# Kernel tuning notes

Hardware: AMD Instinct MI355X
Metric: run time of the kernel (lower is better)

Reference implementation:

```python
import jax, jax.numpy as jnp
import numpy as np

TEMPERATURE = 0.07
NEG = -1e9  # finite stand-in for -inf; exp(-1e9) underflows to 0 in fp32, identical math


def setup_inputs() -> dict:
    key = jax.random.key(0)
    k1, k2 = jax.random.split(key)
    B, D = 8192, 128
    emb = jax.random.normal(k1, (B, D), dtype=jnp.float32)
    emb = emb / jnp.linalg.norm(emb, axis=1, keepdims=True)  # docstring: normalized embeddings
    labels = jax.random.randint(k2, (B,), 0, 2048, dtype=jnp.int64)
    return {"embeddings": emb, "labels": labels}


def reference(embeddings, labels):
    B = labels.shape[0]
    # [B, B] pairwise similarities / temperature
    sim = jnp.matmul(embeddings, embeddings.T) / TEMPERATURE
    eye = jnp.eye(B, dtype=bool)
    sim = jnp.where(eye, NEG, sim)  # mask self-similarity
    # positives: same outfit id, excluding self
    pos_mask = (labels[None, :] == labels[:, None]) & (~eye)
    # row-wise log-softmax (torch code does log_softmax over each row)
    log_probs = jax.nn.log_softmax(sim, axis=1)
    pos_count = jnp.sum(pos_mask, axis=1)  # [B]
    pos_sum = jnp.sum(jnp.where(pos_mask, log_probs, 0.0), axis=1)  # [B]
    has_pos = pos_count > 0
    row_mean = jnp.where(has_pos, pos_sum / jnp.maximum(pos_count, 1), 0.0)
    count = jnp.sum(has_pos)
    loss = -jnp.sum(row_mean) / jnp.maximum(count, 1)
    return loss
```

## Files before the change

kernel.cpp:

```cpp
#include <hip/hip_runtime.h>


#define BATCH 8192
#define DIMK  128
#define INV_T 14.285714285714286f
#define MSUB  14.285714285714286f
#define K1    20.609929155311264f
#define K2    20.609929155311264f

typedef short bf16x8 __attribute__((ext_vector_type(8)));
typedef float f32x4  __attribute__((ext_vector_type(4)));

__device__ __forceinline__ unsigned short f2bf_rne(float f) {
    unsigned u = __float_as_uint(f);
    u += 0x7FFFu + ((u >> 16) & 1u);
    return (unsigned short)(u >> 16);
}
__device__ __forceinline__ float bf2f(unsigned short b) {
    return __uint_as_float(((unsigned)b) << 16);
}

__global__ __launch_bounds__(256) void
prep_kernel(const float* __restrict__ emb, ushort* __restrict__ Ebf,
            float4* __restrict__ zcol4) {
    int i = blockIdx.x * 256 + threadIdx.x;
    if (i < 2048) {
        float4 z = {0.f, 0.f, 0.f, 0.f};
        zcol4[i] = z;
    }
    float4 v = ((const float4*)emb)[i];
    ushort4 o;
    o.x = f2bf_rne(v.x); o.y = f2bf_rne(v.y);
    o.z = f2bf_rne(v.z); o.w = f2bf_rne(v.w);
    ((ushort4*)Ebf)[i] = o;
}

__global__ __launch_bounds__(512) void
contrastive_main(const ushort* __restrict__ Ebf, float* __restrict__ zpartR,
                 float* __restrict__ zcol, const float* __restrict__ emb,
                 const int* __restrict__ labels, float* __restrict__ gsum,
                 int* __restrict__ gcnt) {
    __shared__ __align__(16) ushort Bs[2048 * 8];
    __shared__ float cpart[8][128];
    const int tid  = threadIdx.x;
    const int lane = tid & 63;
    const int wid  = tid >> 6;
    const int quad = lane >> 4;
    const int l16  = lane & 15;

    if (blockIdx.x >= 1056) {
        int* labs = (int*)&Bs[0];
#pragma unroll
        for (int it = 0; it < 4; ++it)
            ((int4*)labs)[it * 512 + tid] = ((const int4*)labels)[it * 512 + tid];
        __syncthreads();

        const int c = (blockIdx.x - 1056) * 8 + wid;
        float2 acc = {0.f, 0.f};
        int cnt = 0;
        int nl = labs[lane];
        for (int j0 = 0; j0 < BATCH; j0 += 64) {
            int cur = nl;
            int nidx = j0 + 64 < BATCH ? j0 + 64 : 0;
            nl = labs[nidx + lane];
            unsigned long long m = __ballot(cur == c);
            cnt += __popcll(m);
            while (m) {
                int j = __ffsll(m) - 1;
                m &= m - 1;
                float2 v = *(const float2*)(emb + (size_t)(j0 + j) * DIMK + lane * 2);
                acc.x += v.x; acc.y += v.y;
            }
        }
        *(float2*)(gsum + (size_t)c * DIMK + lane * 2) = acc;
        if (lane == 0) gcnt[c] = cnt;
        return;
    }

    const int bid = blockIdx.x;
    const int tt  = (bid & 7) * 132 + (bid >> 3);

    int b = tt >> 1;
    const int ch = tt & 1;
    int ti = 0;
    while (b >= 32 - ti) { b -= 32 - ti; ++ti; }
    const int tj  = ti + b;
    const int tj2 = tj * 2 + ch;
    const int row_base = ti * 256 + wid * 32;
    const int col_base = tj * 256 + ch * 128;

    bf16x8 afrag[2][4];
#pragma unroll
    for (int mt = 0; mt < 2; ++mt)
#pragma unroll
        for (int kk = 0; kk < 4; ++kk)
            afrag[mt][kk] = *(const bf16x8*)(Ebf + (size_t)(row_base + mt * 16 + l16) * DIMK
                                             + kk * 32 + quad * 8);

#pragma unroll
    for (int it = 0; it < 4; ++it) {
        int f   = it * 512 + tid;
        int col = f >> 4;
        int c   = f & 15;
        uint4 v = *(const uint4*)(Ebf + (size_t)(col_base + col) * DIMK + c * 8);
        *(uint4*)&Bs[((col >> 4) * 256 + c * 16 + ((col & 15) ^ c)) * 8] = v;
    }
    __syncthreads();

    float zacc[8];
#pragma unroll
    for (int s = 0; s < 8; ++s) zacc[s] = 0.f;

    for (int nt = 0; nt < 8; ++nt) {
        bf16x8 bfrag[4];
#pragma unroll
        for (int kk = 0; kk < 4; ++kk) {
            const int c2 = kk * 4 + quad;
            bfrag[kk] = *(const bf16x8*)&Bs[(nt * 256 + c2 * 16 + (l16 ^ c2)) * 8];
        }

        float csum = 0.f;
#pragma unroll
        for (int mt = 0; mt < 2; ++mt) {
            f32x4 c = {0.f, 0.f, 0.f, 0.f};
#pragma unroll
            for (int kk = 0; kk < 4; ++kk)
                c = __builtin_amdgcn_mfma_f32_16x16x32_bf16(afrag[mt][kk], bfrag[kk], c, 0, 0, 0);
#pragma unroll
            for (int r = 0; r < 4; ++r) {
                float e = __builtin_amdgcn_exp2f(__builtin_fmaf(c[r], K1, -K2));
                zacc[mt * 4 + r] += e;
                csum += e;
            }
        }
        csum += __shfl_xor(csum, 16, 64);
        csum += __shfl_xor(csum, 32, 64);
        if (quad == 0) cpart[wid][nt * 16 + l16] = csum;
    }

#pragma unroll
    for (int s = 0; s < 8; ++s) {
        float z = zacc[s];
#pragma unroll
        for (int m = 1; m <= 8; m <<= 1) z += __shfl_xor(z, m, 64);
        if (l16 == 0) {
            int row = row_base + (s >> 2) * 16 + quad * 4 + (s & 3);
            zpartR[(size_t)row * 64 + tj2] = z;
        }
    }

    __syncthreads();
    if (ti != tj && tid < 128) {
        float s = cpart[0][tid] + cpart[1][tid] + cpart[2][tid] + cpart[3][tid]
                + cpart[4][tid] + cpart[5][tid] + cpart[6][tid] + cpart[7][tid];
        atomicAdd(&zcol[col_base + tid], s);
    }
}

__global__ __launch_bounds__(256) void
finalize1(const float* __restrict__ emb, const ushort* __restrict__ Ebf,
          const int* __restrict__ labels, const float* __restrict__ gsum,
          const int* __restrict__ gcnt, const float* __restrict__ zpartR,
          const float* __restrict__ zcol,
          float* __restrict__ bpart, int* __restrict__ bcnt) {
    __shared__ float sf[4];
    __shared__ int   si[4];
    const int lane = threadIdx.x & 63;
    const int wid  = threadIdx.x >> 6;

    float wsum = 0.f;
    int   wcnt = 0;
#pragma unroll
    for (int it = 0; it < 4; ++it) {
        const int r   = blockIdx.x * 16 + wid * 4 + it;
        const int lab = labels[r];
        const int P   = gcnt[lab] - 1;
        const int tp2 = (r >> 8) * 2;

        float2 ev = *(const float2*)(emb  + (size_t)r   * DIMK + lane * 2);
        float2 gv = *(const float2*)(gsum + (size_t)lab * DIMK + lane * 2);
        unsigned bb = *(const unsigned*)(Ebf + (size_t)r * DIMK + lane * 2);
        float b0 = bf2f((unsigned short)(bb & 0xFFFF));
        float b1 = bf2f((unsigned short)(bb >> 16));

        float dotg = ev.x * gv.x + ev.y * gv.y;
        float ssd  = ev.x * ev.x + ev.y * ev.y;
        float sdbf = b0 * b0 + b1 * b1;
        float Z = 0.f;
        if (lane >= tp2) Z = zpartR[(size_t)r * 64 + lane];

#pragma unroll
        for (int m = 1; m <= 32; m <<= 1) {
            dotg += __shfl_xor(dotg, m, 64);
            ssd  += __shfl_xor(ssd,  m, 64);
            sdbf += __shfl_xor(sdbf, m, 64);
            Z    += __shfl_xor(Z,    m, 64);
        }
        Z += zcol[r];
        Z -= __builtin_amdgcn_exp2f(__builtin_fmaf(sdbf, K1, -K2));

        const bool has = (P > 0);
        wsum += has ? ((dotg - ssd) * INV_T / (float)P - MSUB - __logf(Z)) : 0.f;
        wcnt += has ? 1 : 0;
    }

    if (lane == 0) { sf[wid] = wsum; si[wid] = wcnt; }
    __syncthreads();
    if (threadIdx.x == 0) {
        bpart[blockIdx.x] = sf[0] + sf[1] + sf[2] + sf[3];
        bcnt [blockIdx.x] = si[0] + si[1] + si[2] + si[3];
    }
}

__global__ __launch_bounds__(256) void
finalize2(const float* __restrict__ bpart, const int* __restrict__ bcnt,
          float* __restrict__ out) {
    __shared__ float sf[4];
    __shared__ int   si[4];
    const int t = threadIdx.x;
    float v = 0.f; int c = 0;
#pragma unroll
    for (int k = 0; k < 2; ++k) {
        v += bpart[t + k * 256];
        c += bcnt [t + k * 256];
    }
#pragma unroll
    for (int m = 1; m <= 32; m <<= 1) {
        v += __shfl_xor(v, m, 64);
        c += __shfl_xor(c, m, 64);
    }
    if ((t & 63) == 0) { sf[t >> 6] = v; si[t >> 6] = c; }
    __syncthreads();
    if (t == 0) {
        float tot = sf[0] + sf[1] + sf[2] + sf[3];
        int cc = si[0] + si[1] + si[2] + si[3];
        out[0] = -tot / (float)(cc > 0 ? cc : 1);
    }
}

extern "C" void kernel_launch(void* const* d_in, const int* in_sizes, int n_in,
                              void* d_out, int out_size, void* d_ws, size_t ws_size,
                              hipStream_t stream) {
    const float* emb  = (const float*)d_in[0];
    const int* labels = (const int*)d_in[1];
    float* out        = (float*)d_out;

    char* ws = (char*)d_ws;
    ushort* Ebf    = (ushort*)ws;
    float*  zpartR = (float*)(ws + (2u << 20));
    float*  zcol   = (float*)(ws + (4u << 20));
    float*  gsum   = (float*)(ws + (5u << 20));
    int*    gcnt   = (int*)  (ws + (6u << 20));
    float*  bpart  = (float*)(ws + (6u << 20) + 8192);
    int*    bcnt   = (int*)  (ws + (6u << 20) + 16384);

    prep_kernel<<<1024, 256, 0, stream>>>(emb, Ebf, (float4*)zcol);
    contrastive_main<<<1312, 512, 0, stream>>>(Ebf, zpartR, zcol,
                                               emb, labels, gsum, gcnt);
    finalize1<<<512, 256, 0, stream>>>(emb, Ebf, labels, gsum, gcnt, zpartR, zcol,
                                       bpart, bcnt);
    finalize2<<<1, 256, 0, stream>>>(bpart, bcnt, out);
}
```

Baseline: 93.28 us.

## Fuse bf16 conversion into main kernel and drop prep kernel

New measurement: 97.29 us. 1.04x slower.

```diff
diff --git a/kernel.cpp b/kernel.cpp
--- a/kernel.cpp
+++ b/kernel.cpp
@@ -19,27 +19,19 @@
 __device__ __forceinline__ float bf2f(unsigned short b) {
     return __uint_as_float(((unsigned)b) << 16);
 }
-
-__global__ __launch_bounds__(256) void
-prep_kernel(const float* __restrict__ emb, ushort* __restrict__ Ebf,
-            float4* __restrict__ zcol4) {
-    int i = blockIdx.x * 256 + threadIdx.x;
-    if (i < 2048) {
-        float4 z = {0.f, 0.f, 0.f, 0.f};
-        zcol4[i] = z;
-    }
-    float4 v = ((const float4*)emb)[i];
-    ushort4 o;
-    o.x = f2bf_rne(v.x); o.y = f2bf_rne(v.y);
-    o.z = f2bf_rne(v.z); o.w = f2bf_rne(v.w);
-    ((ushort4*)Ebf)[i] = o;
+__device__ __forceinline__ bf16x8 cvt8(float4 a, float4 b) {
+    bf16x8 o;
+    o[0] = (short)f2bf_rne(a.x); o[1] = (short)f2bf_rne(a.y);
+    o[2] = (short)f2bf_rne(a.z); o[3] = (short)f2bf_rne(a.w);
+    o[4] = (short)f2bf_rne(b.x); o[5] = (short)f2bf_rne(b.y);
+    o[6] = (short)f2bf_rne(b.z); o[7] = (short)f2bf_rne(b.w);
+    return o;
 }
 
 __global__ __launch_bounds__(512) void
-contrastive_main(const ushort* __restrict__ Ebf, float* __restrict__ zpartR,
-                 float* __restrict__ zcol, const float* __restrict__ emb,
-                 const int* __restrict__ labels, float* __restrict__ gsum,
-                 int* __restrict__ gcnt) {
+contrastive_main(const float* __restrict__ emb, const int* __restrict__ labels,
+                 float* __restrict__ zpartR, float* __restrict__ zcol,
+                 float* __restrict__ gsum, int* __restrict__ gcnt) {
     __shared__ __align__(16) ushort Bs[2048 * 8];
     __shared__ float cpart[8][128];
     const int tid  = threadIdx.x;
@@ -93,17 +85,20 @@
 #pragma unroll
     for (int mt = 0; mt < 2; ++mt)
 #pragma unroll
-        for (int kk = 0; kk < 4; ++kk)
-            afrag[mt][kk] = *(const bf16x8*)(Ebf + (size_t)(row_base + mt * 16 + l16) * DIMK
-                                             + kk * 32 + quad * 8);
+        for (int kk = 0; kk < 4; ++kk) {
+            const float* p = emb + (size_t)(row_base + mt * 16 + l16) * DIMK
+                             + kk * 32 + quad * 8;
+            afrag[mt][kk] = cvt8(*(const float4*)p, *(const float4*)(p + 4));
+        }
 
 #pragma unroll
     for (int it = 0; it < 4; ++it) {
         int f   = it * 512 + tid;
         int col = f >> 4;
         int c   = f & 15;
-        uint4 v = *(const uint4*)(Ebf + (size_t)(col_base + col) * DIMK + c * 8);
-        *(uint4*)&Bs[((col >> 4) * 256 + c * 16 + ((col & 15) ^ c)) * 8] = v;
+        const float* p = emb + (size_t)(col_base + col) * DIMK + c * 8;
+        bf16x8 v = cvt8(*(const float4*)p, *(const float4*)(p + 4));
+        *(bf16x8*)&Bs[((col >> 4) * 256 + c * 16 + ((col & 15) ^ c)) * 8] = v;
     }
     __syncthreads();
 
@@ -158,10 +153,9 @@
 }
 
 __global__ __launch_bounds__(256) void
-finalize1(const float* __restrict__ emb, const ushort* __restrict__ Ebf,
-          const int* __restrict__ labels, const float* __restrict__ gsum,
-          const int* __restrict__ gcnt, const float* __restrict__ zpartR,
-          const float* __restrict__ zcol,
+finalize1(const float* __restrict__ emb, const int* __restrict__ labels,
+          const float* __restrict__ gsum, const int* __restrict__ gcnt,
+          const float* __restrict__ zpartR, const float* __restrict__ zcol,
           float* __restrict__ bpart, int* __restrict__ bcnt) {
     __shared__ float sf[4];
     __shared__ int   si[4];
@@ -171,17 +165,16 @@
     float wsum = 0.f;
     int   wcnt = 0;
 #pragma unroll
-    for (int it = 0; it < 4; ++it) {
-        const int r   = blockIdx.x * 16 + wid * 4 + it;
+    for (int it = 0; it < 2; ++it) {
+        const int r   = blockIdx.x * 8 + wid * 2 + it;
         const int lab = labels[r];
         const int P   = gcnt[lab] - 1;
         const int tp2 = (r >> 8) * 2;
 
         float2 ev = *(const float2*)(emb  + (size_t)r   * DIMK + lane * 2);
         float2 gv = *(const float2*)(gsum + (size_t)lab * DIMK + lane * 2);
-        unsigned bb = *(const unsigned*)(Ebf + (size_t)r * DIMK + lane * 2);
-        float b0 = bf2f((unsigned short)(bb & 0xFFFF));
-        float b1 = bf2f((unsigned short)(bb >> 16));
+        float b0 = bf2f(f2bf_rne(ev.x));
+        float b1 = bf2f(f2bf_rne(ev.y));
 
         float dotg = ev.x * gv.x + ev.y * gv.y;
         float ssd  = ev.x * ev.x + ev.y * ev.y;
@@ -220,7 +213,7 @@
     const int t = threadIdx.x;
     float v = 0.f; int c = 0;
 #pragma unroll
-    for (int k = 0; k < 2; ++k) {
+    for (int k = 0; k < 4; ++k) {
         v += bpart[t + k * 256];
         c += bcnt [t + k * 256];
     }
@@ -246,18 +239,17 @@
     float* out        = (float*)d_out;
 
     char* ws = (char*)d_ws;
-    ushort* Ebf    = (ushort*)ws;
-    float*  zpartR = (float*)(ws + (2u << 20));
-    float*  zcol   = (float*)(ws + (4u << 20));
-    float*  gsum   = (float*)(ws + (5u << 20));
-    int*    gcnt   = (int*)  (ws + (6u << 20));
-    float*  bpart  = (float*)(ws + (6u << 20) + 8192);
-    int*    bcnt   = (int*)  (ws + (6u << 20) + 16384);
-
-    prep_kernel<<<1024, 256, 0, stream>>>(emb, Ebf, (float4*)zcol);
-    contrastive_main<<<1312, 512, 0, stream>>>(Ebf, zpartR, zcol,
-                                               emb, labels, gsum, gcnt);
-    finalize1<<<512, 256, 0, stream>>>(emb, Ebf, labels, gsum, gcnt, zpartR, zcol,
-                                       bpart, bcnt);
+    float*  zpartR = (float*)ws;
+    float*  zcol   = (float*)(ws + (2u << 20));
+    float*  gsum   = (float*)(ws + (3u << 20));
+    int*    gcnt   = (int*)  (ws + (4u << 20));
+    float*  bpart  = (float*)(ws + (4u << 20) + 8192);
+    int*    bcnt   = (int*)  (ws + (4u << 20) + 16384);
+
+    hipMemsetAsync(zcol, 0, BATCH * sizeof(float), stream);
+    contrastive_main<<<1312, 512, 0, stream>>>(emb, labels, zpartR, zcol,
+                                               gsum, gcnt);
+    finalize1<<<1024, 256, 0, stream>>>(emb, labels, gsum, gcnt, zpartR, zcol,
+                                        bpart, bcnt);
     finalize2<<<1, 256, 0, stream>>>(bpart, bcnt, out);
 }
```
